# Performance work log

Hardware: AMD Instinct MI355X
Metric: run time of the kernel (lower is better)

## Reference

```python
import jax, jax.numpy as jnp
import numpy as np
from math import sqrt

B, IN_F, OUT_F = 32, 1024, 4096
DROPOUT_RATE = 0.1


def setup_inputs() -> dict:
    key = jax.random.key(0)
    kx, kw, kb, kmw, kmb = jax.random.split(key, 5)
    k = sqrt(1.0 / IN_F)  # He-style init std from source
    x = jax.random.normal(kx, (B, IN_F), dtype=jnp.float32)
    weight = k * jax.random.normal(kw, (IN_F, OUT_F), dtype=jnp.float32)
    bias = k * jax.random.normal(kb, (OUT_F,), dtype=jnp.float32)
    # per-sample Bernoulli keep masks: rand > dropout_rate (no 1/(1-p) rescale in source)
    w_mask = jax.random.uniform(kmw, (B, IN_F, OUT_F)) > DROPOUT_RATE
    b_mask = jax.random.uniform(kmb, (B, OUT_F)) > DROPOUT_RATE
    return {"x": x, "weight": weight, "bias": bias, "w_mask": w_mask, "b_mask": b_mask}


def reference(x, weight, bias, w_mask, b_mask):
    # 'w' dropout mode: per-sample masked weight matmul, vectorized over batch
    # (replaces the original Python loop of B GEMVs with one batched contraction).
    mw = w_mask.astype(x.dtype)
    y = jnp.einsum("bi,io,bio->bo", x, weight, mw)  # [B, OUT_F]
    return y + bias[None, :] * b_mask.astype(x.dtype)
```

## Files before the change

kernel.cpp:

```cpp
#include <hip/hip_runtime.h>


#define B_DIM 32
#define IN_F 1024
#define OUT_F 4096
#define BGRP 8
#define NBG (B_DIM / BGRP)
#define N_CHUNK 32
#define I_CHUNK (IN_F / N_CHUNK)
#define BO (B_DIM * OUT_F)

typedef int   v4i __attribute__((ext_vector_type(4)));
typedef float v4f __attribute__((ext_vector_type(4)));

__global__ __launch_bounds__(256, 2) void masked_gemv_partial(
    const float* __restrict__ x,
    const float* __restrict__ weight,
    const int* __restrict__ w_mask,
    float* __restrict__ partial)
{
    const int bid   = blockIdx.x;
    const int bgrp  = bid >> 7;
    const int o_blk = (bid >> 5) & 3;
    const int chunk = bid & 31;
    const int b0    = bgrp * BGRP;
    const int i0    = chunk * I_CHUNK;
    const int o     = o_blk * 1024 + (threadIdx.x << 2);

    __shared__ float xs[BGRP][I_CHUNK];
    {
        const int bb = threadIdx.x >> 5;
        const int ii = threadIdx.x & 31;
        xs[bb][ii] = x[(b0 + bb) * IN_F + i0 + ii];
    }
    __syncthreads();

    const float* wptr = weight + (size_t)i0 * OUT_F + o;
    const int*   mbase = w_mask + ((size_t)b0 * IN_F + i0) * OUT_F + o;

    v4f acc[BGRP];
#pragma unroll
    for (int bb = 0; bb < BGRP; ++bb) acc[bb] = (v4f){0.f, 0.f, 0.f, 0.f};

#pragma unroll 2
    for (int i = 0; i < I_CHUNK; ++i) {
        const v4f w = *(const v4f*)(wptr + (size_t)i * OUT_F);
#pragma unroll
        for (int bb = 0; bb < BGRP; ++bb) {
            const v4i m = __builtin_nontemporal_load(
                (const v4i*)(mbase + ((size_t)bb * IN_F + i) * OUT_F));
            const float xi = xs[bb][i];
            acc[bb].x = fmaf(xi * (float)m.x, w.x, acc[bb].x);
            acc[bb].y = fmaf(xi * (float)m.y, w.y, acc[bb].y);
            acc[bb].z = fmaf(xi * (float)m.z, w.z, acc[bb].z);
            acc[bb].w = fmaf(xi * (float)m.w, w.w, acc[bb].w);
        }
    }

#pragma unroll
    for (int bb = 0; bb < BGRP; ++bb) {
        __builtin_nontemporal_store(acc[bb],
            (v4f*)(partial + (size_t)chunk * BO + (b0 + bb) * OUT_F + o));
    }
}

__global__ __launch_bounds__(256) void reduce_bias_kernel(
    const float* __restrict__ partial,
    const float* __restrict__ bias,
    const int* __restrict__ b_mask,
    float* __restrict__ out)
{
    const int tid = blockIdx.x * 256 + threadIdx.x;
    const v4f* p4 = (const v4f*)partial;
    v4f s = {0.f, 0.f, 0.f, 0.f};
#pragma unroll
    for (int c = 0; c < N_CHUNK; ++c) {
        const v4f v = p4[(size_t)c * (BO / 4) + tid];
        s.x += v.x; s.y += v.y; s.z += v.z; s.w += v.w;
    }
    const v4i bm = ((const v4i*)b_mask)[tid];
    const v4f bi = ((const v4f*)bias)[tid & (OUT_F / 4 - 1)];
    v4f r;
    r.x = fmaf(bi.x, (float)bm.x, s.x);
    r.y = fmaf(bi.y, (float)bm.y, s.y);
    r.z = fmaf(bi.z, (float)bm.z, s.z);
    r.w = fmaf(bi.w, (float)bm.w, s.w);
    ((v4f*)out)[tid] = r;
}

extern "C" void kernel_launch(void* const* d_in, const int* in_sizes, int n_in,
                              void* d_out, int out_size, void* d_ws, size_t ws_size,
                              hipStream_t stream) {
    const float* x      = (const float*)d_in[0];
    const float* weight = (const float*)d_in[1];
    const float* bias   = (const float*)d_in[2];
    const int*   w_mask = (const int*)d_in[3];
    const int*   b_mask = (const int*)d_in[4];
    float* out     = (float*)d_out;
    float* partial = (float*)d_ws;

    masked_gemv_partial<<<NBG * 4 * N_CHUNK, 256, 0, stream>>>(x, weight, w_mask, partial);
    reduce_bias_kernel<<<BO / 4 / 256, 256, 0, stream>>>(partial, bias, b_mask, out);
}
```

Before: 685.3 us.

## Assign one batch row per block, covering all outputs, with 16 input chunks

```diff
diff --git a/kernel.cpp b/kernel.cpp
--- a/kernel.cpp
+++ b/kernel.cpp
@@ -4,9 +4,7 @@
 #define B_DIM 32
 #define IN_F 1024
 #define OUT_F 4096
-#define BGRP 8
-#define NBG (B_DIM / BGRP)
-#define N_CHUNK 32
+#define N_CHUNK 16
 #define I_CHUNK (IN_F / N_CHUNK)
 #define BO (B_DIM * OUT_F)
 
@@ -20,48 +18,41 @@
     float* __restrict__ partial)
 {
     const int bid   = blockIdx.x;
-    const int bgrp  = bid >> 7;
-    const int o_blk = (bid >> 5) & 3;
-    const int chunk = bid & 31;
-    const int b0    = bgrp * BGRP;
+    const int b     = bid >> 4;
+    const int chunk = bid & 15;
     const int i0    = chunk * I_CHUNK;
-    const int o     = o_blk * 1024 + (threadIdx.x << 2);
 
-    __shared__ float xs[BGRP][I_CHUNK];
-    {
-        const int bb = threadIdx.x >> 5;
-        const int ii = threadIdx.x & 31;
-        xs[bb][ii] = x[(b0 + bb) * IN_F + i0 + ii];
-    }
+    __shared__ float xs[I_CHUNK];
+    if (threadIdx.x < I_CHUNK)
+        xs[threadIdx.x] = x[b * IN_F + i0 + threadIdx.x];
     __syncthreads();
 
-    const float* wptr = weight + (size_t)i0 * OUT_F + o;
-    const int*   mbase = w_mask + ((size_t)b0 * IN_F + i0) * OUT_F + o;
+    const int*   mptr = w_mask + ((size_t)b * IN_F + i0) * OUT_F + (threadIdx.x << 2);
+    const float* wptr = weight + (size_t)i0 * OUT_F + (threadIdx.x << 2);
 
-    v4f acc[BGRP];
+    v4f acc[4];
 #pragma unroll
-    for (int bb = 0; bb < BGRP; ++bb) acc[bb] = (v4f){0.f, 0.f, 0.f, 0.f};
+    for (int q = 0; q < 4; ++q) acc[q] = (v4f){0.f, 0.f, 0.f, 0.f};
 
 #pragma unroll 2
     for (int i = 0; i < I_CHUNK; ++i) {
-        const v4f w = *(const v4f*)(wptr + (size_t)i * OUT_F);
+        const float  xi  = xs[i];
+        const size_t row = (size_t)i * OUT_F;
 #pragma unroll
-        for (int bb = 0; bb < BGRP; ++bb) {
-            const v4i m = __builtin_nontemporal_load(
-                (const v4i*)(mbase + ((size_t)bb * IN_F + i) * OUT_F));
-            const float xi = xs[bb][i];
-            acc[bb].x = fmaf(xi * (float)m.x, w.x, acc[bb].x);
-            acc[bb].y = fmaf(xi * (float)m.y, w.y, acc[bb].y);
-            acc[bb].z = fmaf(xi * (float)m.z, w.z, acc[bb].z);
-            acc[bb].w = fmaf(xi * (float)m.w, w.w, acc[bb].w);
+        for (int q = 0; q < 4; ++q) {
+            const v4i m = *(const v4i*)(mptr + row + q * 1024);
+            const v4f w = *(const v4f*)(wptr + row + q * 1024);
+            acc[q].x = fmaf(xi * (float)m.x, w.x, acc[q].x);
+            acc[q].y = fmaf(xi * (float)m.y, w.y, acc[q].y);
+            acc[q].z = fmaf(xi * (float)m.z, w.z, acc[q].z);
+            acc[q].w = fmaf(xi * (float)m.w, w.w, acc[q].w);
         }
     }
 
+    float* pbase = partial + (size_t)chunk * BO + b * OUT_F + (threadIdx.x << 2);
 #pragma unroll
-    for (int bb = 0; bb < BGRP; ++bb) {
-        __builtin_nontemporal_store(acc[bb],
-            (v4f*)(partial + (size_t)chunk * BO + (b0 + bb) * OUT_F + o));
-    }
+    for (int q = 0; q < 4; ++q)
+        __builtin_nontemporal_store(acc[q], (v4f*)(pbase + q * 1024));
 }
 
 __global__ __launch_bounds__(256) void reduce_bias_kernel(
@@ -99,6 +90,6 @@
     float* out     = (float*)d_out;
     float* partial = (float*)d_ws;
 
-    masked_gemv_partial<<<NBG * 4 * N_CHUNK, 256, 0, stream>>>(x, weight, w_mask, partial);
+    masked_gemv_partial<<<B_DIM * N_CHUNK, 256, 0, stream>>>(x, weight, w_mask, partial);
     reduce_bias_kernel<<<BO / 4 / 256, 256, 0, stream>>>(partial, bias, b_mask, out);
 }
```

After: 690.8 us. About the same (+0.8%).
